# Kernel optimization log

Hardware: AMD Instinct MI355X
Metric: run time of the kernel (lower is better)

The kernel has to match this reference:

```python
import jax, jax.numpy as jnp
import numpy as np

NEG = -1e9


def setup_inputs() -> dict:
    key = jax.random.key(0)
    ks = jax.random.split(key, 9)
    B, L, S, E = 8, 2048, 2048, 1024
    H, G, KD, VD = 16, 64, 1024, 1024
    return {
        "query": jax.random.normal(ks[0], (B, L, E), jnp.float32),
        "key": jax.random.normal(ks[1], (B, S, E), jnp.float32),
        "value": jax.random.normal(ks[2], (B, S, E), jnp.float32),
        "other": jnp.zeros((1,), jnp.float32),
        "key_padding_mask": jax.random.bernoulli(ks[3], 0.1, (B, S)),
        "nhead": H,
        "query_proj": jax.random.normal(ks[4], (1, E, KD), jnp.float32) * 0.02,
        "key_proj": jax.random.normal(ks[5], (1, E, KD), jnp.float32) * 0.02,
        "value_proj": jax.random.normal(ks[6], (1, E, VD), jnp.float32) * 0.02,
        "importance_proj": jax.random.normal(ks[7], (1, E, H * G), jnp.float32) * 0.02,
        "output_proj": jax.random.normal(ks[8], (1, VD, E), jnp.float32) * 0.02,
    }


def reference(query, key, value, other, key_padding_mask, nhead,
              query_proj, key_proj, value_proj, importance_proj, output_proj):
    B, L, E = query.shape
    S = key.shape[1]
    H = nhead
    KD = query_proj.shape[-1]
    VD = value_proj.shape[-1]
    Ek, Ev = KD // H, VD // H
    G = importance_proj.shape[-1] // H
    scale = 1.0 / jnp.sqrt(jnp.asarray(Ek, query.dtype))

    # projections -> (B, H, L/S, d)
    qs = (query @ query_proj[0]).reshape(B, L, H, Ek).transpose(0, 2, 1, 3)
    kk = (key @ key_proj[0]).reshape(B, S, H, Ek).transpose(0, 2, 1, 3)
    vs = (value @ value_proj[0]).reshape(B, S, H, Ev).transpose(0, 2, 1, 3)

    # importance-weighted global queries: softmax over L
    ips = (query @ importance_proj[0]).reshape(B, L, H, G).transpose(0, 2, 3, 1)  # (B,H,G,L)
    ips = jax.nn.softmax(ips, axis=-1)
    gqs = jnp.einsum('bhgl,bhld->bhgd', ips, qs)  # (B,H,G,Ek)

    # stage 1: global queries attend over all keys (shared attn for keys & values)
    g_scores = jnp.einsum('bhgd,bhsd->bhgs', gqs, kk) * scale  # (B,H,G,S)
    g_scores = jnp.where(key_padding_mask[:, None, None, :], NEG, g_scores)
    g_attn = jax.nn.softmax(g_scores, axis=-1)
    global_keys = jnp.einsum('bhgs,bhsd->bhgd', g_attn, kk)   # (B,H,G,Ek)
    global_values = jnp.einsum('bhgs,bhsd->bhgd', g_attn, vs)  # (B,H,G,Ev)

    # stage 2: local queries attend over G global keys/values
    l_scores = jnp.einsum('bhld,bhgd->bhlg', qs, global_keys) * scale  # (B,H,L,G)
    l_attn = jax.nn.softmax(l_scores, axis=-1)
    out = jnp.einsum('bhlg,bhgd->bhld', l_attn, global_values)  # (B,H,L,Ev)

    out = out.transpose(0, 2, 1, 3).reshape(B, L, H * Ev)
    out = out @ output_proj[0]  # (B,L,E)
    return (out, l_attn)
```

## Files before the change

### kernel.cpp

```cpp
#include <hip/hip_runtime.h>


typedef float f32x4 __attribute__((ext_vector_type(4)));
typedef _Float16 f16x8 __attribute__((ext_vector_type(8)));
typedef unsigned short u16;

#define DEV static __device__ __forceinline__

DEV u16 f2h(float x){
  _Float16 h = (_Float16)x;
  return __builtin_bit_cast(u16, h);
}
DEV float h2f(u16 u){
  return (float)__builtin_bit_cast(_Float16, u);
}
DEV void split1h(float x, u16 &h, u16 &l){
  h = f2h(x);
  l = f2h(x - h2f(h));
}
DEV unsigned pk2h(float a, float b){
  return (unsigned)f2h(a) | ((unsigned)f2h(b) << 16);
}

DEV void gload16(const u16* src, u16* dst_lds){
  __builtin_amdgcn_global_load_lds(
      (__attribute__((address_space(1))) void*)src,
      (__attribute__((address_space(3))) void*)dst_lds, 16, 0, 0);
}

__global__ __launch_bounds__(256)
void mask_norm(const unsigned char* __restrict__ src, unsigned char* __restrict__ dst, int n)
{
  const unsigned* w = (const unsigned*)src;
  const int tid = threadIdx.x;
  int local = 0;
  for (int i = tid; i < n/4; i += 256){
    unsigned v = w[i];
    if (v == 0x3F800000u) local |= 2;
    else if (v > 1u)      local |= 1;
  }
  __shared__ int red[256];
  red[tid] = local;
  __syncthreads();
  for (int s = 128; s; s >>= 1){
    if (tid < s) red[tid] |= red[tid+s];
    __syncthreads();
  }
  const int r = red[0];
  const int mode = (r & 2) ? 2 : ((r & 1) ? 1 : 0);
  for (int i = tid; i < n; i += 256){
    unsigned char v;
    if (mode == 1) v = src[i] ? 1 : 0;
    else           v = w[i]   ? 1 : 0;
    dst[i] = v;
  }
}

__global__ __launch_bounds__(256)
void conv_hi(const float* __restrict__ x, u16* __restrict__ hi, int n8)
{
  const int i = blockIdx.x*256 + threadIdx.x;
  if (i >= n8) return;
  f32x4 a = ((const f32x4*)x)[2*i], b = ((const f32x4*)x)[2*i+1];
  uint4 uh;
  uh.x = pk2h(a[0], a[1]); uh.y = pk2h(a[2], a[3]);
  uh.z = pk2h(b[0], b[1]); uh.w = pk2h(b[2], b[3]);
  ((uint4*)hi)[i] = uh;
}

__global__ __launch_bounds__(256)
void transpose_hi(const float* __restrict__ Wsrc, u16* __restrict__ Whi, int Kd, int Nd)
{
  __shared__ float t[64][65];
  const int tid = threadIdx.x;
  const int n0 = blockIdx.x * 64, k0 = blockIdx.y * 64;
  #pragma unroll
  for (int it = 0; it < 16; ++it){
    int e = it*256 + tid, r = e >> 6, c = e & 63;
    t[r][c] = Wsrc[(long)(k0+r)*Nd + (n0+c)];
  }
  __syncthreads();
  #pragma unroll
  for (int it = 0; it < 16; ++it){
    int e = it*256 + tid, r = e >> 6, c = e & 63;
    Whi[(long)(n0+r)*Kd + (k0+c)] = f2h(t[c][r]);
  }
}

template<int TM, int TERMS, int CM, int EPI, int SWZ>
__global__ __launch_bounds__(256)
void gemm_g(const u16* __restrict__ Ah_g, const u16* __restrict__ Al_g,
            const u16* __restrict__ Bh_g,
            void* __restrict__ Cp, void* __restrict__ Cp2,
            const unsigned char* __restrict__ maskp,
            int K, int lda, int ldb, int ldc,
            long aB, long aH, long bB, long bH, long cB, long cH,
            int H2, int Ssz, float scale)
{
  constexpr int BN = 128, BK = 32;
  constexpr int WM = TM/2, WN = BN/2;
  constexpr int FM = WM/16, FN = WN/16;
  __shared__ __align__(16) u16 AhS[2][TM*BK];
  __shared__ __align__(16) u16 AlS[2][TERMS == 2 ? TM*BK : 8];
  __shared__ __align__(16) u16 BhS[2][BN*BK];

  const int tid = threadIdx.x;
  int bx = blockIdx.x, by = blockIdx.y;
  if constexpr (SWZ){
    const int gx = gridDim.x;
    const int nwg = gx * gridDim.y;
    const int q = nwg >> 3;
    const int flat = bx + gx * by;
    const int nf = (flat & 7) * q + (flat >> 3);
    bx = nf % gx; by = nf / gx;
  }
  const int batch = blockIdx.z;
  const int b = batch / H2, h = batch - b*H2;
  const long aOff = (long)b*aB + (long)h*aH;
  const long bOff = (long)b*bB + (long)h*bH;
  const long cOff = (long)b*cB + (long)h*cH;
  const int nBase = bx * BN;
  const int mBase = by * TM;
  const int wave = tid >> 6, lane = tid & 63;
  const int wm = wave >> 1, wn = wave & 1;
  const int cg8 = (lane & 3) * 8;
  const int rsub = lane >> 2;

  auto stage = [&](int buf, int k0){
    #pragma unroll
    for (int c = 0; c < TM/64; ++c){
      const int chunk = wave*(TM/64) + c;
      const long g = aOff + (long)(mBase + chunk*16 + rsub)*lda + k0 + cg8;
      gload16(Ah_g + g, &AhS[buf][chunk*512]);
      if constexpr (TERMS == 2) gload16(Al_g + g, &AlS[buf][chunk*512]);
    }
    #pragma unroll
    for (int c = 0; c < 2; ++c){
      const int chunk = wave*2 + c;
      const long g = bOff + (long)(nBase + chunk*16 + rsub)*ldb + k0 + cg8;
      gload16(Bh_g + g, &BhS[buf][chunk*512]);
    }
  };

  f32x4 acc[FM][FN] = {};

  stage(0, 0);
  __syncthreads();
  const int nk = K >> 5;
  for (int t = 0; t < nk; ++t){
    const int buf = t & 1;
    if (t + 1 < nk) stage(buf ^ 1, (t + 1) << 5);

    f16x8 ah[FM], al[FM], bh[FN];
    #pragma unroll
    for (int mi = 0; mi < FM; ++mi){
      const int off = (wm*WM + mi*16 + (lane & 15))*BK + (lane >> 4)*8;
      ah[mi] = *(const f16x8*)&AhS[buf][off];
      if constexpr (TERMS == 2) al[mi] = *(const f16x8*)&AlS[buf][off];
    }
    #pragma unroll
    for (int ni = 0; ni < FN; ++ni){
      const int off = (wn*WN + ni*16 + (lane & 15))*BK + (lane >> 4)*8;
      bh[ni] = *(const f16x8*)&BhS[buf][off];
    }
    #pragma unroll
    for (int mi = 0; mi < FM; ++mi)
      #pragma unroll
      for (int ni = 0; ni < FN; ++ni){
        acc[mi][ni] = __builtin_amdgcn_mfma_f32_16x16x32_f16(ah[mi], bh[ni], acc[mi][ni], 0, 0, 0);
        if constexpr (TERMS == 2)
          acc[mi][ni] = __builtin_amdgcn_mfma_f32_16x16x32_f16(al[mi], bh[ni], acc[mi][ni], 0, 0, 0);
      }
    __syncthreads();
  }

  const int cr = (lane >> 4) * 4, cc = lane & 15;
  #pragma unroll
  for (int mi = 0; mi < FM; ++mi)
    #pragma unroll
    for (int ni = 0; ni < FN; ++ni)
      #pragma unroll
      for (int r = 0; r < 4; ++r){
        const int row = mBase + wm*WM + mi*16 + cr + r;
        const int col = nBase + wn*WN + ni*16 + cc;
        float v = acc[mi][ni][r];
        if constexpr (EPI == 1){
          v *= scale;
          if (maskp[(long)b*Ssz + col]) v = -50000.0f;
        }
        const long ci = cOff + (long)row*ldc + col;
        if constexpr (CM == 0){
          ((float*)Cp)[ci] = v;
        } else {
          u16 hh, ll;
          split1h(v, hh, ll);
          ((u16*)Cp)[ci]  = hh;
          ((u16*)Cp2)[ci] = ll;
        }
      }
}

__global__ __launch_bounds__(256)
void softmax_split(u16* __restrict__ hi, u16* __restrict__ lo)
{
  const long base = (long)blockIdx.x * 2048;
  const int tid = threadIdx.x;
  const int lane = tid & 63, wv = tid >> 6;
  uint4 uh = ((const uint4*)(hi + base))[tid];
  uint4 ul = ((const uint4*)(lo + base))[tid];
  float v[8];
  v[0] = h2f((u16)uh.x) + h2f((u16)ul.x);
  v[1] = h2f((u16)(uh.x>>16)) + h2f((u16)(ul.x>>16));
  v[2] = h2f((u16)uh.y) + h2f((u16)ul.y);
  v[3] = h2f((u16)(uh.y>>16)) + h2f((u16)(ul.y>>16));
  v[4] = h2f((u16)uh.z) + h2f((u16)ul.z);
  v[5] = h2f((u16)(uh.z>>16)) + h2f((u16)(ul.z>>16));
  v[6] = h2f((u16)uh.w) + h2f((u16)ul.w);
  v[7] = h2f((u16)(uh.w>>16)) + h2f((u16)(ul.w>>16));
  float m = v[0];
  #pragma unroll
  for (int i = 1; i < 8; ++i) m = fmaxf(m, v[i]);
  #pragma unroll
  for (int off = 32; off; off >>= 1) m = fmaxf(m, __shfl_xor(m, off));
  __shared__ float rm[4], rs[4];
  if (lane == 0) rm[wv] = m;
  __syncthreads();
  m = fmaxf(fmaxf(rm[0],rm[1]), fmaxf(rm[2],rm[3]));
  float s = 0.f;
  #pragma unroll
  for (int i = 0; i < 8; ++i){ v[i] = __expf(v[i]-m); s += v[i]; }
  #pragma unroll
  for (int off = 32; off; off >>= 1) s += __shfl_xor(s, off);
  if (lane == 0) rs[wv] = s;
  __syncthreads();
  s = (rs[0]+rs[1]) + (rs[2]+rs[3]);
  const float inv = 1.0f / s;
  u16 hh[8], ll[8];
  #pragma unroll
  for (int i = 0; i < 8; ++i) split1h(v[i]*inv, hh[i], ll[i]);
  uh.x = (unsigned)hh[0] | ((unsigned)hh[1]<<16);
  uh.y = (unsigned)hh[2] | ((unsigned)hh[3]<<16);
  uh.z = (unsigned)hh[4] | ((unsigned)hh[5]<<16);
  uh.w = (unsigned)hh[6] | ((unsigned)hh[7]<<16);
  ul.x = (unsigned)ll[0] | ((unsigned)ll[1]<<16);
  ul.y = (unsigned)ll[2] | ((unsigned)ll[3]<<16);
  ul.z = (unsigned)ll[4] | ((unsigned)ll[5]<<16);
  ul.w = (unsigned)ll[6] | ((unsigned)ll[7]<<16);
  ((uint4*)(hi + base))[tid] = uh;
  ((uint4*)(lo + base))[tid] = ul;
}

template<int NB>
__global__ __launch_bounds__(256)
void einsum_m(const u16* __restrict__ Ah_g, const u16* __restrict__ Al_g,
              const u16* __restrict__ B1h_g, const u16* __restrict__ B1l_g,
              const u16* __restrict__ B2h_g, const u16* __restrict__ B2l_g,
              float* __restrict__ P1, float* __restrict__ P2,
              int K, int KC, int lda, int ldb,
              long aB, long aH, long bB, long bH, int H2, int nbatch)
{
  __shared__ __align__(16) u16 AhS[64][72];
  __shared__ __align__(16) u16 AlS[64][72];
  __shared__ __align__(16) u16 B1hS[64][72];
  __shared__ __align__(16) u16 B1lS[64][72];
  __shared__ __align__(16) u16 B2hS[NB==2?64:1][72];
  __shared__ __align__(16) u16 B2lS[NB==2?64:1][72];
  const int tid = threadIdx.x;
  const int kc = blockIdx.x, batch = blockIdx.y;
  const int b = batch / H2, h = batch - b*H2;
  const long aOff = (long)b*aB + (long)h*aH;
  const long bOff = (long)b*bB + (long)h*bH;
  const int kchunk = K / KC, kbeg = kc * kchunk;
  const int wm = tid >> 6, lane = tid & 63;
  const int ar = tid >> 3, as = (tid & 7) * 8;

  f32x4 acc1[4] = {};
  f32x4 acc2[4] = {};

  for (int ks = kbeg; ks < kbeg + kchunk; ks += 64){
    if (ks != kbeg) __syncthreads();
    #pragma unroll
    for (int it = 0; it < 2; ++it){
      const int g = it*32 + ar;
      const long ga = aOff + (long)g*lda + ks + as;
      *(uint4*)&AhS[g][as] = *(const uint4*)(Ah_g + ga);
      *(uint4*)&AlS[g][as] = *(const uint4*)(Al_g + ga);
    }
    #pragma unroll
    for (int it = 0; it < 4; ++it){
      const int e = it*256 + tid;
      const int lr = e >> 4, d0 = (e & 15) * 4;
      const long gm = bOff + (long)(ks + lr)*ldb + d0;
      ushort4 h4 = *(const ushort4*)(B1h_g + gm);
      ushort4 l4 = *(const ushort4*)(B1l_g + gm);
      B1hS[d0+0][lr]=h4.x; B1hS[d0+1][lr]=h4.y; B1hS[d0+2][lr]=h4.z; B1hS[d0+3][lr]=h4.w;
      B1lS[d0+0][lr]=l4.x; B1lS[d0+1][lr]=l4.y; B1lS[d0+2][lr]=l4.z; B1lS[d0+3][lr]=l4.w;
      if constexpr (NB == 2){
        ushort4 h42 = *(const ushort4*)(B2h_g + gm);
        ushort4 l42 = *(const ushort4*)(B2l_g + gm);
        B2hS[d0+0][lr]=h42.x; B2hS[d0+1][lr]=h42.y; B2hS[d0+2][lr]=h42.z; B2hS[d0+3][lr]=h42.w;
        B2lS[d0+0][lr]=l42.x; B2lS[d0+1][lr]=l42.y; B2lS[d0+2][lr]=l42.z; B2lS[d0+3][lr]=l42.w;
      }
    }
    __syncthreads();
    #pragma unroll
    for (int k0 = 0; k0 < 64; k0 += 32){
      const int ko = k0 + (lane >> 4)*8;
      const int fr = lane & 15;
      f16x8 a_h = *(const f16x8*)&AhS[wm*16 + fr][ko];
      f16x8 a_l = *(const f16x8*)&AlS[wm*16 + fr][ko];
      #pragma unroll
      for (int ni = 0; ni < 4; ++ni){
        f16x8 b_h = *(const f16x8*)&B1hS[ni*16 + fr][ko];
        f16x8 b_l = *(const f16x8*)&B1lS[ni*16 + fr][ko];
        acc1[ni] = __builtin_amdgcn_mfma_f32_16x16x32_f16(a_h, b_h, acc1[ni], 0, 0, 0);
        acc1[ni] = __builtin_amdgcn_mfma_f32_16x16x32_f16(a_l, b_h, acc1[ni], 0, 0, 0);
        acc1[ni] = __builtin_amdgcn_mfma_f32_16x16x32_f16(a_h, b_l, acc1[ni], 0, 0, 0);
        if constexpr (NB == 2){
          f16x8 c_h = *(const f16x8*)&B2hS[ni*16 + fr][ko];
          f16x8 c_l = *(const f16x8*)&B2lS[ni*16 + fr][ko];
          acc2[ni] = __builtin_amdgcn_mfma_f32_16x16x32_f16(a_h, c_h, acc2[ni], 0, 0, 0);
          acc2[ni] = __builtin_amdgcn_mfma_f32_16x16x32_f16(a_l, c_h, acc2[ni], 0, 0, 0);
          acc2[ni] = __builtin_amdgcn_mfma_f32_16x16x32_f16(a_h, c_l, acc2[ni], 0, 0, 0);
        }
      }
    }
  }
  const long po = ((long)(kc*nbatch + batch) << 12);
  const int cr = (lane >> 4) * 4, cc = lane & 15;
  #pragma unroll
  for (int ni = 0; ni < 4; ++ni)
    #pragma unroll
    for (int r = 0; r < 4; ++r){
      const int g = wm*16 + cr + r, d = ni*16 + cc;
      P1[po + g*64 + d] = acc1[ni][r];
      if constexpr (NB == 2) P2[po + g*64 + d] = acc2[ni][r];
    }
}

__global__ __launch_bounds__(256)
void reduce64(const float* __restrict__ part,
              u16* __restrict__ outhi, u16* __restrict__ outlo,
              int n4, int parts)
{
  const int idx = blockIdx.x*256 + threadIdx.x;
  if (idx >= n4) return;
  f32x4 s = ((const f32x4*)part)[idx];
  for (int p = 1; p < parts; ++p) s += ((const f32x4*)part)[(long)p*n4 + idx];
  ushort4 uh, ul;
  split1h(s[0], uh.x, ul.x); split1h(s[1], uh.y, ul.y);
  split1h(s[2], uh.z, ul.z); split1h(s[3], uh.w, ul.w);
  ((ushort4*)outhi)[idx] = uh;
  ((ushort4*)outlo)[idx] = ul;
}

__global__ __launch_bounds__(256)
void stage2_mfma(const u16* __restrict__ qhi, const u16* __restrict__ qlo,
                 const u16* __restrict__ gkh_g, const u16* __restrict__ gkl_g,
                 const u16* __restrict__ gvh_g, const u16* __restrict__ gvl_g,
                 float* __restrict__ lattn, u16* __restrict__ ahi,
                 float scale)
{
  __shared__ __align__(16) u16 Ah[128][72];
  __shared__ __align__(16) u16 Al[128][72];
  __shared__ __align__(16) u16 Bh[64][72];
  __shared__ __align__(16) u16 Bl[64][72];
  const int tid = threadIdx.x;
  const int bh = blockIdx.y;
  const int b = bh >> 4, h = bh & 15;
  const int l0 = blockIdx.x * 128;
  const int wm = tid >> 6, lane = tid & 63;

  const long qbase = ((long)b*2048 + l0)*1024 + h*64;
  #pragma unroll
  for (int it = 0; it < 4; ++it){
    const int e = it*256 + tid, row = e >> 3, s = e & 7;
    const long g = qbase + (long)row*1024 + s*8;
    *(uint4*)&Ah[row][s*8] = *(const uint4*)(qhi + g);
    *(uint4*)&Al[row][s*8] = *(const uint4*)(qlo + g);
  }
  const long gb = (long)bh * 4096;
  #pragma unroll
  for (int it = 0; it < 2; ++it){
    const int e = it*256 + tid, gr = e >> 3, s = e & 7;
    *(uint4*)&Bh[gr][s*8] = *(const uint4*)(gkh_g + gb + gr*64 + s*8);
    *(uint4*)&Bl[gr][s*8] = *(const uint4*)(gkl_g + gb + gr*64 + s*8);
  }
  __syncthreads();

  f32x4 acc[2][4] = {};
  #pragma unroll
  for (int k0 = 0; k0 < 64; k0 += 32){
    f16x8 a_h[2], a_l[2], b_h[4], b_l[4];
    #pragma unroll
    for (int mi = 0; mi < 2; ++mi){
      const int row = wm*32 + mi*16 + (lane & 15);
      a_h[mi] = *(const f16x8*)&Ah[row][k0 + (lane >> 4)*8];
      a_l[mi] = *(const f16x8*)&Al[row][k0 + (lane >> 4)*8];
    }
    #pragma unroll
    for (int ni = 0; ni < 4; ++ni){
      const int nr = ni*16 + (lane & 15);
      b_h[ni] = *(const f16x8*)&Bh[nr][k0 + (lane >> 4)*8];
      b_l[ni] = *(const f16x8*)&Bl[nr][k0 + (lane >> 4)*8];
    }
    #pragma unroll
    for (int mi = 0; mi < 2; ++mi)
      #pragma unroll
      for (int ni = 0; ni < 4; ++ni){
        acc[mi][ni] = __builtin_amdgcn_mfma_f32_16x16x32_f16(a_h[mi], b_h[ni], acc[mi][ni], 0, 0, 0);
        acc[mi][ni] = __builtin_amdgcn_mfma_f32_16x16x32_f16(a_l[mi], b_h[ni], acc[mi][ni], 0, 0, 0);
        acc[mi][ni] = __builtin_amdgcn_mfma_f32_16x16x32_f16(a_h[mi], b_l[ni], acc[mi][ni], 0, 0, 0);
      }
  }
  __syncthreads();

  #pragma unroll
  for (int it = 0; it < 4; ++it){
    const int e = it*256 + tid;
    const int gr = e >> 4, d0 = (e & 15) * 4;
    ushort4 vh = *(const ushort4*)(gvh_g + gb + gr*64 + d0);
    ushort4 vl = *(const ushort4*)(gvl_g + gb + gr*64 + d0);
    Bh[d0+0][gr] = vh.x; Bh[d0+1][gr] = vh.y; Bh[d0+2][gr] = vh.z; Bh[d0+3][gr] = vh.w;
    Bl[d0+0][gr] = vl.x; Bl[d0+1][gr] = vl.y; Bl[d0+2][gr] = vl.z; Bl[d0+3][gr] = vl.w;
  }

  #pragma unroll
  for (int mi = 0; mi < 2; ++mi){
    #pragma unroll
    for (int r = 0; r < 4; ++r){
      float v0 = acc[mi][0][r]*scale, v1 = acc[mi][1][r]*scale;
      float v2 = acc[mi][2][r]*scale, v3 = acc[mi][3][r]*scale;
      float mx = fmaxf(fmaxf(v0,v1), fmaxf(v2,v3));
      #pragma unroll
      for (int off = 1; off < 16; off <<= 1) mx = fmaxf(mx, __shfl_xor(mx, off, 16));
      float e0 = __expf(v0-mx), e1 = __expf(v1-mx), e2 = __expf(v2-mx), e3 = __expf(v3-mx);
      float sum = (e0+e1) + (e2+e3);
      #pragma unroll
      for (int off = 1; off < 16; off <<= 1) sum += __shfl_xor(sum, off, 16);
      const float inv = 1.0f / sum;
      e0 *= inv; e1 *= inv; e2 *= inv; e3 *= inv;
      const int lrow = wm*32 + mi*16 + (lane >> 4)*4 + r;
      float* lp = lattn + ((long)bh*2048 + l0 + lrow)*64 + (lane & 15);
      lp[0] = e0; lp[16] = e1; lp[32] = e2; lp[48] = e3;
      u16 hh, ll;
      split1h(e0, hh, ll); Ah[lrow][ 0 + (lane&15)] = hh; Al[lrow][ 0 + (lane&15)] = ll;
      split1h(e1, hh, ll); Ah[lrow][16 + (lane&15)] = hh; Al[lrow][16 + (lane&15)] = ll;
      split1h(e2, hh, ll); Ah[lrow][32 + (lane&15)] = hh; Al[lrow][32 + (lane&15)] = ll;
      split1h(e3, hh, ll); Ah[lrow][48 + (lane&15)] = hh; Al[lrow][48 + (lane&15)] = ll;
    }
  }
  __syncthreads();

  f32x4 o[2][4] = {};
  #pragma unroll
  for (int k0 = 0; k0 < 64; k0 += 32){
    f16x8 p_h[2], p_l[2], b_h[4], b_l[4];
    #pragma unroll
    for (int mi = 0; mi < 2; ++mi){
      const int row = wm*32 + mi*16 + (lane & 15);
      p_h[mi] = *(const f16x8*)&Ah[row][k0 + (lane >> 4)*8];
      p_l[mi] = *(const f16x8*)&Al[row][k0 + (lane >> 4)*8];
    }
    #pragma unroll
    for (int ni = 0; ni < 4; ++ni){
      const int nr = ni*16 + (lane & 15);
      b_h[ni] = *(const f16x8*)&Bh[nr][k0 + (lane >> 4)*8];
      b_l[ni] = *(const f16x8*)&Bl[nr][k0 + (lane >> 4)*8];
    }
    #pragma unroll
    for (int mi = 0; mi < 2; ++mi)
      #pragma unroll
      for (int ni = 0; ni < 4; ++ni){
        o[mi][ni] = __builtin_amdgcn_mfma_f32_16x16x32_f16(p_h[mi], b_h[ni], o[mi][ni], 0, 0, 0);
        o[mi][ni] = __builtin_amdgcn_mfma_f32_16x16x32_f16(p_l[mi], b_h[ni], o[mi][ni], 0, 0, 0);
        o[mi][ni] = __builtin_amdgcn_mfma_f32_16x16x32_f16(p_h[mi], b_l[ni], o[mi][ni], 0, 0, 0);
      }
  }

  #pragma unroll
  for (int mi = 0; mi < 2; ++mi)
    #pragma unroll
    for (int ni = 0; ni < 4; ++ni)
      #pragma unroll
      for (int r = 0; r < 4; ++r){
        const int lrow = wm*32 + mi*16 + (lane >> 4)*4 + r;
        const int d = ni*16 + (lane & 15);
        const long oidx = ((long)b*2048 + l0 + lrow)*1024 + h*64 + d;
        ahi[oidx] = f2h(o[mi][ni][r]);
      }
}

extern "C" void kernel_launch(void* const* d_in, const int* in_sizes, int n_in,
                              void* d_out, int out_size, void* d_ws, size_t ws_size,
                              hipStream_t stream)
{
  const float* query = (const float*)d_in[0];
  const float* key   = (const float*)d_in[1];
  const float* value = (const float*)d_in[2];
  const unsigned char* mask_raw = (const unsigned char*)d_in[4];
  const float* Wq = (const float*)d_in[6];
  const float* Wk = (const float*)d_in[7];
  const float* Wv = (const float*)d_in[8];
  const float* Wi = (const float*)d_in[9];
  const float* Wo = (const float*)d_in[10];
  float* out0 = (float*)d_out;
  float* out1 = out0 + 16777216;

  char* ws = (char*)d_ws;
  u16* WoT_hi = (u16*)(ws + 0);
  u16* WqT_hi = (u16*)(ws + (4L<<20));
  u16* WkT_hi = (u16*)(ws + (8L<<20));
  u16* WvT_hi = (u16*)(ws + (12L<<20));
  u16* WiT_hi = (u16*)(ws + (18L<<20));
  unsigned char* mask_ws = (unsigned char*)(ws + (6L<<20));
  u16* gqs_hi = (u16*)(ws + (16L<<20));
  u16* gqs_lo = (u16*)(ws + (17L<<20));
  float* part1 = (float*)(ws + (4L<<20));
  float* part2 = (float*)(ws + (12L<<20));
  u16* qp_hi = (u16*)(ws + (20L<<20));
  u16* kp_hi = qp_hi;
  u16* vp_hi = qp_hi;
  u16* gsc_hi = (u16*)(ws + (20L<<20));
  u16* gsc_lo = (u16*)(ws + (52L<<20));
  u16* qs_hi  = (u16*)(ws + (84L<<20));
  u16* qs_lo  = (u16*)(ws + (116L<<20));
  float* partg = (float*)(ws + (148L<<20));
  u16* vs_hi  = (u16*)(ws + (148L<<20));
  u16* vs_lo  = (u16*)(ws + (180L<<20));
  u16* ips_hi = (u16*)(ws + (212L<<20));
  u16* ips_lo = (u16*)(ws + (244L<<20));
  u16* kk_hi  = (u16*)(ws + (212L<<20));
  u16* kk_lo  = (u16*)(ws + (244L<<20));
  u16* gk_hi  = (u16*)(ws + (212L<<20));
  u16* gk_lo  = (u16*)(ws + (213L<<20));
  u16* gv_hi  = (u16*)(ws + (214L<<20));
  u16* gv_lo  = (u16*)(ws + (215L<<20));
  u16* attn_hi = (u16*)(ws + (244L<<20));

  const dim3 blk(256);
  const float scale = 0.125f;

  transpose_hi<<<dim3(16,16), blk, 0, stream>>>(Wq, WqT_hi, 1024, 1024);
  transpose_hi<<<dim3(16,16), blk, 0, stream>>>(Wk, WkT_hi, 1024, 1024);
  transpose_hi<<<dim3(16,16), blk, 0, stream>>>(Wv, WvT_hi, 1024, 1024);
  transpose_hi<<<dim3(16,16), blk, 0, stream>>>(Wi, WiT_hi, 1024, 1024);
  transpose_hi<<<dim3(16,16), blk, 0, stream>>>(Wo, WoT_hi, 1024, 1024);

  conv_hi<<<8192, blk, 0, stream>>>(query, qp_hi, 2097152);

  gemm_g<128,1,1,0,1><<<dim3(8,128,1), blk, 0, stream>>>(
      qp_hi, nullptr, WqT_hi, qs_hi, qs_lo, nullptr,
      1024, 1024,1024,1024, 0,0, 0,0, 0,0, 1, 2048, 1.f);

  gemm_g<128,1,1,0,0><<<dim3(16,8,8), blk, 0, stream>>>(
      WiT_hi, nullptr, qp_hi, ips_hi, ips_lo, nullptr,
      1024, 1024,1024,2048, 0,0, 2097152L,0, 2097152L,0, 1, 2048, 1.f);
  mask_norm<<<1, blk, 0, stream>>>(mask_raw, mask_ws, 16384);
  softmax_split<<<8192, blk, 0, stream>>>(ips_hi, ips_lo);

  einsum_m<1><<<dim3(4,128), blk, 0, stream>>>(
      ips_hi, ips_lo, qs_hi, qs_lo, nullptr, nullptr, partg, nullptr,
      2048, 4, 2048, 1024, 2097152L, 131072L, 2097152L, 64L, 16, 128);
  reduce64<<<512, blk, 0, stream>>>(partg, gqs_hi, gqs_lo, 131072, 4);

  conv_hi<<<8192, blk, 0, stream>>>(key, kp_hi, 2097152);
  gemm_g<128,1,1,0,1><<<dim3(8,128,1), blk, 0, stream>>>(
      kp_hi, nullptr, WkT_hi, kk_hi, kk_lo, nullptr,
      1024, 1024,1024,1024, 0,0, 0,0, 0,0, 1, 2048, 1.f);

  conv_hi<<<8192, blk, 0, stream>>>(value, vp_hi, 2097152);
  gemm_g<128,1,1,0,1><<<dim3(8,128,1), blk, 0, stream>>>(
      vp_hi, nullptr, WvT_hi, vs_hi, vs_lo, nullptr,
      1024, 1024,1024,1024, 0,0, 0,0, 0,0, 1, 2048, 1.f);

  gemm_g<64,2,1,1,0><<<dim3(16,1,128), blk, 0, stream>>>(
      gqs_hi, gqs_lo, kk_hi, gsc_hi, gsc_lo, mask_ws,
      64, 64,1024,2048, 65536L,4096L, 2097152L,64L, 2097152L,131072L, 16, 2048, scale);
  softmax_split<<<8192, blk, 0, stream>>>(gsc_hi, gsc_lo);

  einsum_m<2><<<dim3(4,128), blk, 0, stream>>>(
      gsc_hi, gsc_lo, kk_hi, kk_lo, vs_hi, vs_lo, part1, part2,
      2048, 4, 2048, 1024, 2097152L, 131072L, 2097152L, 64L, 16, 128);
  reduce64<<<512, blk, 0, stream>>>(part1, gk_hi, gk_lo, 131072, 4);
  reduce64<<<512, blk, 0, stream>>>(part2, gv_hi, gv_lo, 131072, 4);

  stage2_mfma<<<dim3(16,128), blk, 0, stream>>>(qs_hi, qs_lo, gk_hi, gk_lo,
      gv_hi, gv_lo, out1, attn_hi, scale);

  gemm_g<128,1,0,0,1><<<dim3(8,128,1), blk, 0, stream>>>(
      attn_hi, nullptr, WoT_hi, out0, nullptr, nullptr,
      1024, 1024,1024,1024, 0,0, 0,0, 0,0, 1, 2048, 1.f);

  (void)in_sizes; (void)n_in; (void)out_size; (void)ws_size;
}
```

Baseline: 576.5 us.

## Triple-buffer GEMM LDS staging with explicit vmcnt waits

Converts the generic GEMM's double-buffered global-to-LDS loads into a three-stage ring, issuing loads two K-steps ahead and waiting with explicit s_waitcnt vmcnt counts instead of a full __syncthreads. This is meant to hide global memory latency better by keeping more loads in flight. In exchange it uses 1.5x the LDS, which may reduce occupancy, and it adds sched_barriers that constrain the compiler's instruction scheduling.

Result: slower. 597.0 us (+3.6%).

```diff
diff --git a/kernel.cpp b/kernel.cpp
--- a/kernel.cpp
+++ b/kernel.cpp
@@ -26,6 +26,10 @@
   __builtin_amdgcn_global_load_lds(
       (__attribute__((address_space(1))) void*)src,
       (__attribute__((address_space(3))) void*)dst_lds, 16, 0, 0);
+}
+
+template<int N> DEV void wait_vm(){
+  asm volatile("s_waitcnt vmcnt(%0)" :: "i"(N) : "memory");
 }
 
 __global__ __launch_bounds__(256)
@@ -100,9 +104,10 @@
   constexpr int BN = 128, BK = 32;
   constexpr int WM = TM/2, WN = BN/2;
   constexpr int FM = WM/16, FN = WN/16;
-  __shared__ __align__(16) u16 AhS[2][TM*BK];
-  __shared__ __align__(16) u16 AlS[2][TERMS == 2 ? TM*BK : 8];
-  __shared__ __align__(16) u16 BhS[2][BN*BK];
+  constexpr int PL = TM/64 + (TERMS == 2 ? TM/64 : 0) + 2;
+  __shared__ __align__(16) u16 AhS[3][TM*BK];
+  __shared__ __align__(16) u16 AlS[3][TERMS == 2 ? TM*BK : 8];
+  __shared__ __align__(16) u16 BhS[3][BN*BK];
 
   const int tid = threadIdx.x;
   int bx = blockIdx.x, by = blockIdx.y;
@@ -144,25 +149,39 @@
 
   f32x4 acc[FM][FN] = {};
 
+  const int nk = K >> 5;
   stage(0, 0);
-  __syncthreads();
-  const int nk = K >> 5;
+  if (nk > 1) stage(1, 32);
+
+  int cur = 0;
   for (int t = 0; t < nk; ++t){
-    const int buf = t & 1;
-    if (t + 1 < nk) stage(buf ^ 1, (t + 1) << 5);
+    if (t + 2 < nk){
+      int nb = cur + 2; if (nb >= 3) nb -= 3;
+      stage(nb, (t + 2) << 5);
+      wait_vm<2*PL>();
+    } else if (t + 1 < nk){
+      wait_vm<PL>();
+    } else {
+      wait_vm<0>();
+    }
+    __builtin_amdgcn_s_barrier();
+    __builtin_amdgcn_sched_barrier(0);
 
     f16x8 ah[FM], al[FM], bh[FN];
     #pragma unroll
     for (int mi = 0; mi < FM; ++mi){
       const int off = (wm*WM + mi*16 + (lane & 15))*BK + (lane >> 4)*8;
-      ah[mi] = *(const f16x8*)&AhS[buf][off];
-      if constexpr (TERMS == 2) al[mi] = *(const f16x8*)&AlS[buf][off];
+      ah[mi] = *(const f16x8*)&AhS[cur][off];
+      if constexpr (TERMS == 2) al[mi] = *(const f16x8*)&AlS[cur][off];
     }
     #pragma unroll
     for (int ni = 0; ni < FN; ++ni){
       const int off = (wn*WN + ni*16 + (lane & 15))*BK + (lane >> 4)*8;
-      bh[ni] = *(const f16x8*)&BhS[buf][off];
-    }
+      bh[ni] = *(const f16x8*)&BhS[cur][off];
+    }
+    asm volatile("s_waitcnt lgkmcnt(0)" ::: "memory");
+    __builtin_amdgcn_sched_barrier(0);
+
     #pragma unroll
     for (int mi = 0; mi < FM; ++mi)
       #pragma unroll
@@ -171,7 +190,10 @@
         if constexpr (TERMS == 2)
           acc[mi][ni] = __builtin_amdgcn_mfma_f32_16x16x32_f16(al[mi], bh[ni], acc[mi][ni], 0, 0, 0);
       }
-    __syncthreads();
+
+    __builtin_amdgcn_s_barrier();
+    __builtin_amdgcn_sched_barrier(0);
+    ++cur; if (cur >= 3) cur -= 3;
   }
 
   const int cr = (lane >> 4) * 4, cc = lane & 15;
```

## Fuse softmax into aggregation einsums with online-softmax split-K combine

Applied to the files above, without the earlier changes.

Replaces the separate softmax_split pass plus einsum and reduce64 kernels with a flash-style aggregation kernel. It computes a running max and sum per row, rescales the accumulators, and writes partial stats that a small combine kernel merges across two K-chunks. This removes a full read and write of the large score tensors and two extra launches. The five weight transposes and two input conversions are also batched into single launches via blockIdx.z. In exchange, the number of K-splits per batch drops from 4 to 2, so fewer blocks are in flight, and extra syncs are added per tile.

Measured after the change: 565.3 us. About the same (-1.9%).

```diff
diff --git a/kernel.cpp b/kernel.cpp
--- a/kernel.cpp
+++ b/kernel.cpp
@@ -57,8 +57,11 @@
 }
 
 __global__ __launch_bounds__(256)
-void conv_hi(const float* __restrict__ x, u16* __restrict__ hi, int n8)
-{
+void conv_hi2(const float* __restrict__ x0, u16* __restrict__ h0,
+              const float* __restrict__ x1, u16* __restrict__ h1, int n8)
+{
+  const float* x = blockIdx.z ? x1 : x0;
+  u16* hi = blockIdx.z ? h1 : h0;
   const int i = blockIdx.x*256 + threadIdx.x;
   if (i >= n8) return;
   f32x4 a = ((const f32x4*)x)[2*i], b = ((const f32x4*)x)[2*i+1];
@@ -69,21 +72,40 @@
 }
 
 __global__ __launch_bounds__(256)
-void transpose_hi(const float* __restrict__ Wsrc, u16* __restrict__ Whi, int Kd, int Nd)
-{
+void conv_hi(const float* __restrict__ x, u16* __restrict__ hi, int n8)
+{
+  const int i = blockIdx.x*256 + threadIdx.x;
+  if (i >= n8) return;
+  f32x4 a = ((const f32x4*)x)[2*i], b = ((const f32x4*)x)[2*i+1];
+  uint4 uh;
+  uh.x = pk2h(a[0], a[1]); uh.y = pk2h(a[2], a[3]);
+  uh.z = pk2h(b[0], b[1]); uh.w = pk2h(b[2], b[3]);
+  ((uint4*)hi)[i] = uh;
+}
+
+__global__ __launch_bounds__(256)
+void transpose_hi5(const float* __restrict__ s0, const float* __restrict__ s1,
+                   const float* __restrict__ s2, const float* __restrict__ s3,
+                   const float* __restrict__ s4,
+                   u16* __restrict__ d0, u16* __restrict__ d1, u16* __restrict__ d2,
+                   u16* __restrict__ d3, u16* __restrict__ d4)
+{
+  const int z = blockIdx.z;
+  const float* Wsrc = z == 0 ? s0 : z == 1 ? s1 : z == 2 ? s2 : z == 3 ? s3 : s4;
+  u16* Whi = z == 0 ? d0 : z == 1 ? d1 : z == 2 ? d2 : z == 3 ? d3 : d4;
   __shared__ float t[64][65];
   const int tid = threadIdx.x;
   const int n0 = blockIdx.x * 64, k0 = blockIdx.y * 64;
   #pragma unroll
   for (int it = 0; it < 16; ++it){
     int e = it*256 + tid, r = e >> 6, c = e & 63;
-    t[r][c] = Wsrc[(long)(k0+r)*Nd + (n0+c)];
+    t[r][c] = Wsrc[(long)(k0+r)*1024 + (n0+c)];
   }
   __syncthreads();
   #pragma unroll
   for (int it = 0; it < 16; ++it){
     int e = it*256 + tid, r = e >> 6, c = e & 63;
-    Whi[(long)(n0+r)*Kd + (k0+c)] = f2h(t[c][r]);
+    Whi[(long)(n0+r)*1024 + (k0+c)] = f2h(t[c][r]);
   }
 }
 
@@ -200,71 +222,21 @@
       }
 }
 
-__global__ __launch_bounds__(256)
-void softmax_split(u16* __restrict__ hi, u16* __restrict__ lo)
-{
-  const long base = (long)blockIdx.x * 2048;
-  const int tid = threadIdx.x;
-  const int lane = tid & 63, wv = tid >> 6;
-  uint4 uh = ((const uint4*)(hi + base))[tid];
-  uint4 ul = ((const uint4*)(lo + base))[tid];
-  float v[8];
-  v[0] = h2f((u16)uh.x) + h2f((u16)ul.x);
-  v[1] = h2f((u16)(uh.x>>16)) + h2f((u16)(ul.x>>16));
-  v[2] = h2f((u16)uh.y) + h2f((u16)ul.y);
-  v[3] = h2f((u16)(uh.y>>16)) + h2f((u16)(ul.y>>16));
-  v[4] = h2f((u16)uh.z) + h2f((u16)ul.z);
-  v[5] = h2f((u16)(uh.z>>16)) + h2f((u16)(ul.z>>16));
-  v[6] = h2f((u16)uh.w) + h2f((u16)ul.w);
-  v[7] = h2f((u16)(uh.w>>16)) + h2f((u16)(ul.w>>16));
-  float m = v[0];
-  #pragma unroll
-  for (int i = 1; i < 8; ++i) m = fmaxf(m, v[i]);
-  #pragma unroll
-  for (int off = 32; off; off >>= 1) m = fmaxf(m, __shfl_xor(m, off));
-  __shared__ float rm[4], rs[4];
-  if (lane == 0) rm[wv] = m;
-  __syncthreads();
-  m = fmaxf(fmaxf(rm[0],rm[1]), fmaxf(rm[2],rm[3]));
-  float s = 0.f;
-  #pragma unroll
-  for (int i = 0; i < 8; ++i){ v[i] = __expf(v[i]-m); s += v[i]; }
-  #pragma unroll
-  for (int off = 32; off; off >>= 1) s += __shfl_xor(s, off);
-  if (lane == 0) rs[wv] = s;
-  __syncthreads();
-  s = (rs[0]+rs[1]) + (rs[2]+rs[3]);
-  const float inv = 1.0f / s;
-  u16 hh[8], ll[8];
-  #pragma unroll
-  for (int i = 0; i < 8; ++i) split1h(v[i]*inv, hh[i], ll[i]);
-  uh.x = (unsigned)hh[0] | ((unsigned)hh[1]<<16);
-  uh.y = (unsigned)hh[2] | ((unsigned)hh[3]<<16);
-  uh.z = (unsigned)hh[4] | ((unsigned)hh[5]<<16);
-  uh.w = (unsigned)hh[6] | ((unsigned)hh[7]<<16);
-  ul.x = (unsigned)ll[0] | ((unsigned)ll[1]<<16);
-  ul.y = (unsigned)ll[2] | ((unsigned)ll[3]<<16);
-  ul.z = (unsigned)ll[4] | ((unsigned)ll[5]<<16);
-  ul.w = (unsigned)ll[6] | ((unsigned)ll[7]<<16);
-  ((uint4*)(hi + base))[tid] = uh;
-  ((uint4*)(lo + base))[tid] = ul;
-}
-
 template<int NB>
 __global__ __launch_bounds__(256)
-void einsum_m(const u16* __restrict__ Ah_g, const u16* __restrict__ Al_g,
-              const u16* __restrict__ B1h_g, const u16* __restrict__ B1l_g,
-              const u16* __restrict__ B2h_g, const u16* __restrict__ B2l_g,
-              float* __restrict__ P1, float* __restrict__ P2,
-              int K, int KC, int lda, int ldb,
-              long aB, long aH, long bB, long bH, int H2, int nbatch)
-{
-  __shared__ __align__(16) u16 AhS[64][72];
-  __shared__ __align__(16) u16 AlS[64][72];
-  __shared__ __align__(16) u16 B1hS[64][72];
-  __shared__ __align__(16) u16 B1lS[64][72];
-  __shared__ __align__(16) u16 B2hS[NB==2?64:1][72];
-  __shared__ __align__(16) u16 B2lS[NB==2?64:1][72];
+void flash_agg(const u16* __restrict__ Sh_g, const u16* __restrict__ Sl_g,
+               const u16* __restrict__ B1h_g, const u16* __restrict__ B1l_g,
+               const u16* __restrict__ B2h_g, const u16* __restrict__ B2l_g,
+               float* __restrict__ P1, float* __restrict__ P2,
+               float* __restrict__ msm, float* __restrict__ mss,
+               int K, int KC, int lda, int ldb,
+               long aB, long aH, long bB, long bH, int H2, int nbatch)
+{
+  __shared__ __align__(16) u16 Ah[64][72], Al[64][72];
+  __shared__ __align__(16) u16 Ph[64][72], Pl[64][72];
+  __shared__ __align__(16) u16 B1h[64][72], B1l[64][72];
+  __shared__ __align__(16) u16 B2h[NB==2?64:1][72], B2l[NB==2?64:1][72];
+  __shared__ float mS[64], sS[64], fS[64];
   const int tid = threadIdx.x;
   const int kc = blockIdx.x, batch = blockIdx.y;
   const int b = batch / H2, h = batch - b*H2;
@@ -272,19 +244,20 @@
   const long bOff = (long)b*bB + (long)h*bH;
   const int kchunk = K / KC, kbeg = kc * kchunk;
   const int wm = tid >> 6, lane = tid & 63;
-  const int ar = tid >> 3, as = (tid & 7) * 8;
-
-  f32x4 acc1[4] = {};
-  f32x4 acc2[4] = {};
+  const int srow = tid >> 2, sq = tid & 3;
+
+  if (tid < 64){ mS[tid] = -1e30f; sS[tid] = 0.f; }
+
+  f32x4 acc1[4] = {}, acc2[4] = {};
 
   for (int ks = kbeg; ks < kbeg + kchunk; ks += 64){
-    if (ks != kbeg) __syncthreads();
+    __syncthreads();
     #pragma unroll
     for (int it = 0; it < 2; ++it){
-      const int g = it*32 + ar;
-      const long ga = aOff + (long)g*lda + ks + as;
-      *(uint4*)&AhS[g][as] = *(const uint4*)(Ah_g + ga);
-      *(uint4*)&AlS[g][as] = *(const uint4*)(Al_g + ga);
+      const int e = it*256 + tid, row = e >> 3, c8 = (e & 7) * 8;
+      const long ga = aOff + (long)row*lda + ks + c8;
+      *(uint4*)&Ah[row][c8] = *(const uint4*)(Sh_g + ga);
+      *(uint4*)&Al[row][c8] = *(const uint4*)(Sl_g + ga);
     }
     #pragma unroll
     for (int it = 0; it < 4; ++it){
@@ -293,32 +266,98 @@
       const long gm = bOff + (long)(ks + lr)*ldb + d0;
       ushort4 h4 = *(const ushort4*)(B1h_g + gm);
       ushort4 l4 = *(const ushort4*)(B1l_g + gm);
-      B1hS[d0+0][lr]=h4.x; B1hS[d0+1][lr]=h4.y; B1hS[d0+2][lr]=h4.z; B1hS[d0+3][lr]=h4.w;
-      B1lS[d0+0][lr]=l4.x; B1lS[d0+1][lr]=l4.y; B1lS[d0+2][lr]=l4.z; B1lS[d0+3][lr]=l4.w;
+      B1h[d0+0][lr]=h4.x; B1h[d0+1][lr]=h4.y; B1h[d0+2][lr]=h4.z; B1h[d0+3][lr]=h4.w;
+      B1l[d0+0][lr]=l4.x; B1l[d0+1][lr]=l4.y; B1l[d0+2][lr]=l4.z; B1l[d0+3][lr]=l4.w;
       if constexpr (NB == 2){
         ushort4 h42 = *(const ushort4*)(B2h_g + gm);
         ushort4 l42 = *(const ushort4*)(B2l_g + gm);
-        B2hS[d0+0][lr]=h42.x; B2hS[d0+1][lr]=h42.y; B2hS[d0+2][lr]=h42.z; B2hS[d0+3][lr]=h42.w;
-        B2lS[d0+0][lr]=l42.x; B2lS[d0+1][lr]=l42.y; B2lS[d0+2][lr]=l42.z; B2lS[d0+3][lr]=l42.w;
+        B2h[d0+0][lr]=h42.x; B2h[d0+1][lr]=h42.y; B2h[d0+2][lr]=h42.z; B2h[d0+3][lr]=h42.w;
+        B2l[d0+0][lr]=l42.x; B2l[d0+1][lr]=l42.y; B2l[d0+2][lr]=l42.z; B2l[d0+3][lr]=l42.w;
       }
     }
     __syncthreads();
+
+    float v[16];
+    {
+      uint4 ha = *(const uint4*)&Ah[srow][sq*16];
+      uint4 hb = *(const uint4*)&Ah[srow][sq*16 + 8];
+      uint4 la = *(const uint4*)&Al[srow][sq*16];
+      uint4 lb = *(const uint4*)&Al[srow][sq*16 + 8];
+      v[0]=h2f((u16)ha.x)+h2f((u16)la.x);  v[1]=h2f((u16)(ha.x>>16))+h2f((u16)(la.x>>16));
+      v[2]=h2f((u16)ha.y)+h2f((u16)la.y);  v[3]=h2f((u16)(ha.y>>16))+h2f((u16)(la.y>>16));
+      v[4]=h2f((u16)ha.z)+h2f((u16)la.z);  v[5]=h2f((u16)(ha.z>>16))+h2f((u16)(la.z>>16));
+      v[6]=h2f((u16)ha.w)+h2f((u16)la.w);  v[7]=h2f((u16)(ha.w>>16))+h2f((u16)(la.w>>16));
+      v[8]=h2f((u16)hb.x)+h2f((u16)lb.x);  v[9]=h2f((u16)(hb.x>>16))+h2f((u16)(lb.x>>16));
+      v[10]=h2f((u16)hb.y)+h2f((u16)lb.y); v[11]=h2f((u16)(hb.y>>16))+h2f((u16)(lb.y>>16));
+      v[12]=h2f((u16)hb.z)+h2f((u16)lb.z); v[13]=h2f((u16)(hb.z>>16))+h2f((u16)(lb.z>>16));
+      v[14]=h2f((u16)hb.w)+h2f((u16)lb.w); v[15]=h2f((u16)(hb.w>>16))+h2f((u16)(lb.w>>16));
+    }
+    float mx = v[0];
+    #pragma unroll
+    for (int i = 1; i < 16; ++i) mx = fmaxf(mx, v[i]);
+    mx = fmaxf(mx, __shfl_xor(mx, 1));
+    mx = fmaxf(mx, __shfl_xor(mx, 2));
+    const float mold = mS[srow];
+    const float mnew = fmaxf(mold, mx);
+    float sum = 0.f;
+    u16 ph[16], pl[16];
+    #pragma unroll
+    for (int i = 0; i < 16; ++i){
+      float e = __expf(v[i] - mnew);
+      sum += e;
+      split1h(e, ph[i], pl[i]);
+    }
+    sum += __shfl_xor(sum, 1);
+    sum += __shfl_xor(sum, 2);
+    if (sq == 0){
+      const float f = __expf(mold - mnew);
+      sS[srow] = sS[srow] * f + sum;
+      mS[srow] = mnew;
+      fS[srow] = f;
+    }
+    {
+      uint4 uh0, uh1, ul0, ul1;
+      uh0.x=(unsigned)ph[0]|((unsigned)ph[1]<<16);  uh0.y=(unsigned)ph[2]|((unsigned)ph[3]<<16);
+      uh0.z=(unsigned)ph[4]|((unsigned)ph[5]<<16);  uh0.w=(unsigned)ph[6]|((unsigned)ph[7]<<16);
+      uh1.x=(unsigned)ph[8]|((unsigned)ph[9]<<16);  uh1.y=(unsigned)ph[10]|((unsigned)ph[11]<<16);
+      uh1.z=(unsigned)ph[12]|((unsigned)ph[13]<<16);uh1.w=(unsigned)ph[14]|((unsigned)ph[15]<<16);
+      ul0.x=(unsigned)pl[0]|((unsigned)pl[1]<<16);  ul0.y=(unsigned)pl[2]|((unsigned)pl[3]<<16);
+      ul0.z=(unsigned)pl[4]|((unsigned)pl[5]<<16);  ul0.w=(unsigned)pl[6]|((unsigned)pl[7]<<16);
+      ul1.x=(unsigned)pl[8]|((unsigned)pl[9]<<16);  ul1.y=(unsigned)pl[10]|((unsigned)pl[11]<<16);
+      ul1.z=(unsigned)pl[12]|((unsigned)pl[13]<<16);ul1.w=(unsigned)pl[14]|((unsigned)pl[15]<<16);
+      *(uint4*)&Ph[srow][sq*16]     = uh0;
+      *(uint4*)&Ph[srow][sq*16 + 8] = uh1;
+      *(uint4*)&Pl[srow][sq*16]     = ul0;
+      *(uint4*)&Pl[srow][sq*16 + 8] = ul1;
+    }
+    __syncthreads();
+
+    float fr4[4];
+    #pragma unroll
+    for (int r = 0; r < 4; ++r) fr4[r] = fS[wm*16 + (lane >> 4)*4 + r];
+    #pragma unroll
+    for (int ni = 0; ni < 4; ++ni)
+      #pragma unroll
+      for (int r = 0; r < 4; ++r){
+        acc1[ni][r] *= fr4[r];
+        if constexpr (NB == 2) acc2[ni][r] *= fr4[r];
+      }
     #pragma unroll
     for (int k0 = 0; k0 < 64; k0 += 32){
       const int ko = k0 + (lane >> 4)*8;
       const int fr = lane & 15;
-      f16x8 a_h = *(const f16x8*)&AhS[wm*16 + fr][ko];
-      f16x8 a_l = *(const f16x8*)&AlS[wm*16 + fr][ko];
+      f16x8 a_h = *(const f16x8*)&Ph[wm*16 + fr][ko];
+      f16x8 a_l = *(const f16x8*)&Pl[wm*16 + fr][ko];
       #pragma unroll
       for (int ni = 0; ni < 4; ++ni){
-        f16x8 b_h = *(const f16x8*)&B1hS[ni*16 + fr][ko];
-        f16x8 b_l = *(const f16x8*)&B1lS[ni*16 + fr][ko];
+        f16x8 b_h = *(const f16x8*)&B1h[ni*16 + fr][ko];
+        f16x8 b_l = *(const f16x8*)&B1l[ni*16 + fr][ko];
         acc1[ni] = __builtin_amdgcn_mfma_f32_16x16x32_f16(a_h, b_h, acc1[ni], 0, 0, 0);
         acc1[ni] = __builtin_amdgcn_mfma_f32_16x16x32_f16(a_l, b_h, acc1[ni], 0, 0, 0);
         acc1[ni] = __builtin_amdgcn_mfma_f32_16x16x32_f16(a_h, b_l, acc1[ni], 0, 0, 0);
         if constexpr (NB == 2){
-          f16x8 c_h = *(const f16x8*)&B2hS[ni*16 + fr][ko];
-          f16x8 c_l = *(const f16x8*)&B2lS[ni*16 + fr][ko];
+          f16x8 c_h = *(const f16x8*)&B2h[ni*16 + fr][ko];
+          f16x8 c_l = *(const f16x8*)&B2l[ni*16 + fr][ko];
           acc2[ni] = __builtin_amdgcn_mfma_f32_16x16x32_f16(a_h, c_h, acc2[ni], 0, 0, 0);
           acc2[ni] = __builtin_amdgcn_mfma_f32_16x16x32_f16(a_l, c_h, acc2[ni], 0, 0, 0);
           acc2[ni] = __builtin_amdgcn_mfma_f32_16x16x32_f16(a_h, c_l, acc2[ni], 0, 0, 0);
@@ -326,6 +365,7 @@
       }
     }
   }
+
   const long po = ((long)(kc*nbatch + batch) << 12);
   const int cr = (lane >> 4) * 4, cc = lane & 15;
   #pragma unroll
@@ -336,22 +376,61 @@
       P1[po + g*64 + d] = acc1[ni][r];
       if constexpr (NB == 2) P2[po + g*64 + d] = acc2[ni][r];
     }
-}
-
-__global__ __launch_bounds__(256)
-void reduce64(const float* __restrict__ part,
-              u16* __restrict__ outhi, u16* __restrict__ outlo,
-              int n4, int parts)
-{
-  const int idx = blockIdx.x*256 + threadIdx.x;
-  if (idx >= n4) return;
-  f32x4 s = ((const f32x4*)part)[idx];
-  for (int p = 1; p < parts; ++p) s += ((const f32x4*)part)[(long)p*n4 + idx];
-  ushort4 uh, ul;
-  split1h(s[0], uh.x, ul.x); split1h(s[1], uh.y, ul.y);
-  split1h(s[2], uh.z, ul.z); split1h(s[3], uh.w, ul.w);
-  ((ushort4*)outhi)[idx] = uh;
-  ((ushort4*)outlo)[idx] = ul;
+  if (tid < 64){
+    msm[((long)kc*nbatch + batch)*64 + tid] = mS[tid];
+    mss[((long)kc*nbatch + batch)*64 + tid] = sS[tid];
+  }
+}
+
+template<int NB>
+__global__ __launch_bounds__(256)
+void flash_combine(const float* __restrict__ P1, const float* __restrict__ P2,
+                   const float* __restrict__ msm, const float* __restrict__ mss,
+                   u16* __restrict__ o1h, u16* __restrict__ o1l,
+                   u16* __restrict__ o2h, u16* __restrict__ o2l, int nbatch)
+{
+  const int batch = blockIdx.x;
+  const int tid = threadIdx.x;
+  const int g = tid >> 2, dq = (tid & 3) * 16;
+  const float m0 = msm[(long)batch*64 + g];
+  const float m1 = msm[((long)nbatch + batch)*64 + g];
+  const float s0 = mss[(long)batch*64 + g];
+  const float s1 = mss[((long)nbatch + batch)*64 + g];
+  const float M = fmaxf(m0, m1);
+  float w0 = __expf(m0 - M), w1 = __expf(m1 - M);
+  const float inv = 1.0f / (s0*w0 + s1*w1);
+  w0 *= inv; w1 *= inv;
+  const long i0 = ((long)batch << 12) + g*64 + dq;
+  const long i1 = (((long)nbatch + batch) << 12) + g*64 + dq;
+  const long oo = (long)batch*4096 + g*64 + dq;
+  #pragma unroll
+  for (int nb = 0; nb < NB; ++nb){
+    const float* Pa = nb ? P2 : P1;
+    u16* oh = nb ? o2h : o1h;
+    u16* ol = nb ? o2l : o1l;
+    u16 hh[16], ll[16];
+    #pragma unroll
+    for (int j = 0; j < 4; ++j){
+      f32x4 a = *(const f32x4*)(Pa + i0 + j*4);
+      f32x4 c = *(const f32x4*)(Pa + i1 + j*4);
+      #pragma unroll
+      for (int e = 0; e < 4; ++e)
+        split1h(a[e]*w0 + c[e]*w1, hh[j*4+e], ll[j*4+e]);
+    }
+    uint4 uh0, uh1, ul0, ul1;
+    uh0.x=(unsigned)hh[0]|((unsigned)hh[1]<<16);  uh0.y=(unsigned)hh[2]|((unsigned)hh[3]<<16);
+    uh0.z=(unsigned)hh[4]|((unsigned)hh[5]<<16);  uh0.w=(unsigned)hh[6]|((unsigned)hh[7]<<16);
+    uh1.x=(unsigned)hh[8]|((unsigned)hh[9]<<16);  uh1.y=(unsigned)hh[10]|((unsigned)hh[11]<<16);
+    uh1.z=(unsigned)hh[12]|((unsigned)hh[13]<<16);uh1.w=(unsigned)hh[14]|((unsigned)hh[15]<<16);
+    ul0.x=(unsigned)ll[0]|((unsigned)ll[1]<<16);  ul0.y=(unsigned)ll[2]|((unsigned)ll[3]<<16);
+    ul0.z=(unsigned)ll[4]|((unsigned)ll[5]<<16);  ul0.w=(unsigned)ll[6]|((unsigned)ll[7]<<16);
+    ul1.x=(unsigned)ll[8]|((unsigned)ll[9]<<16);  ul1.y=(unsigned)ll[10]|((unsigned)ll[11]<<16);
+    ul1.z=(unsigned)ll[12]|((unsigned)ll[13]<<16);ul1.w=(unsigned)ll[14]|((unsigned)ll[15]<<16);
+    *(uint4*)(oh + oo)     = uh0;
+    *(uint4*)(oh + oo + 8) = uh1;
+    *(uint4*)(ol + oo)     = ul0;
+    *(uint4*)(ol + oo + 8) = ul1;
+  }
 }
 
 __global__ __launch_bounds__(256)
@@ -509,19 +588,23 @@
 
   char* ws = (char*)d_ws;
   u16* WoT_hi = (u16*)(ws + 0);
+  float* msm_q = (float*)(ws + (2L<<20));
+  float* mss_q = (float*)(ws + (2L<<20) + 262144);
+  float* msm_g = (float*)(ws + (3L<<20));
+  float* mss_g = (float*)(ws + (3L<<20) + 262144);
   u16* WqT_hi = (u16*)(ws + (4L<<20));
+  unsigned char* mask_ws = (unsigned char*)(ws + (6L<<20));
+  float* part1 = (float*)(ws + (4L<<20));
   u16* WkT_hi = (u16*)(ws + (8L<<20));
   u16* WvT_hi = (u16*)(ws + (12L<<20));
-  u16* WiT_hi = (u16*)(ws + (18L<<20));
-  unsigned char* mask_ws = (unsigned char*)(ws + (6L<<20));
+  float* part2 = (float*)(ws + (12L<<20));
   u16* gqs_hi = (u16*)(ws + (16L<<20));
   u16* gqs_lo = (u16*)(ws + (17L<<20));
-  float* part1 = (float*)(ws + (4L<<20));
-  float* part2 = (float*)(ws + (12L<<20));
-  u16* qp_hi = (u16*)(ws + (20L<<20));
-  u16* kp_hi = qp_hi;
-  u16* vp_hi = qp_hi;
+  u16* WiT_hi = (u16*)(ws + (18L<<20));
+  u16* qp_hi  = (u16*)(ws + (20L<<20));
+  u16* vp_hi  = qp_hi;
   u16* gsc_hi = (u16*)(ws + (20L<<20));
+  u16* kp_hi  = (u16*)(ws + (52L<<20));
   u16* gsc_lo = (u16*)(ws + (52L<<20));
   u16* qs_hi  = (u16*)(ws + (84L<<20));
   u16* qs_lo  = (u16*)(ws + (116L<<20));
@@ -541,13 +624,12 @@
   const dim3 blk(256);
   const float scale = 0.125f;
 
-  transpose_hi<<<dim3(16,16), blk, 0, stream>>>(Wq, WqT_hi, 1024, 1024);
-  transpose_hi<<<dim3(16,16), blk, 0, stream>>>(Wk, WkT_hi, 1024, 1024);
-  transpose_hi<<<dim3(16,16), blk, 0, stream>>>(Wv, WvT_hi, 1024, 1024);
-  transpose_hi<<<dim3(16,16), blk, 0, stream>>>(Wi, WiT_hi, 1024, 1024);
-  transpose_hi<<<dim3(16,16), blk, 0, stream>>>(Wo, WoT_hi, 1024, 1024);
-
-  conv_hi<<<8192, blk, 0, stream>>>(query, qp_hi, 2097152);
+  mask_norm<<<1, blk, 0, stream>>>(mask_raw, mask_ws, 16384);
+
+  transpose_hi5<<<dim3(16,16,5), blk, 0, stream>>>(Wq, Wk, Wv, Wi, Wo,
+      WqT_hi, WkT_hi, WvT_hi, WiT_hi, WoT_hi);
+
+  conv_hi2<<<dim3(8192,1,2), blk, 0, stream>>>(query, qp_hi, key, kp_hi, 2097152);
 
   gemm_g<128,1,1,0,1><<<dim3(8,128,1), blk, 0, stream>>>(
       qp_hi, nullptr, WqT_hi, qs_hi, qs_lo, nullptr,
@@ -556,15 +638,14 @@
   gemm_g<128,1,1,0,0><<<dim3(16,8,8), blk, 0, stream>>>(
       WiT_hi, nullptr, qp_hi, ips_hi, ips_lo, nullptr,
       1024, 1024,1024,2048, 0,0, 2097152L,0, 2097152L,0, 1, 2048, 1.f);
-  mask_norm<<<1, blk, 0, stream>>>(mask_raw, mask_ws, 16384);
-  softmax_split<<<8192, blk, 0, stream>>>(ips_hi, ips_lo);
-
-  einsum_m<1><<<dim3(4,128), blk, 0, stream>>>(
-      ips_hi, ips_lo, qs_hi, qs_lo, nullptr, nullptr, partg, nullptr,
-      2048, 4, 2048, 1024, 2097152L, 131072L, 2097152L, 64L, 16, 128);
-  reduce64<<<512, blk, 0, stream>>>(partg, gqs_hi, gqs_lo, 131072, 4);
-
-  conv_hi<<<8192, blk, 0, stream>>>(key, kp_hi, 2097152);
+
+  flash_agg<1><<<dim3(2,128), blk, 0, stream>>>(
+      ips_hi, ips_lo, qs_hi, qs_lo, nullptr, nullptr,
+      partg, nullptr, msm_q, mss_q,
+      2048, 2, 2048, 1024, 2097152L, 131072L, 2097152L, 64L, 16, 128);
+  flash_combine<1><<<128, blk, 0, stream>>>(
+      partg, nullptr, msm_q, mss_q, gqs_hi, gqs_lo, nullptr, nullptr, 128);
+
   gemm_g<128,1,1,0,1><<<dim3(8,128,1), blk, 0, stream>>>(
       kp_hi, nullptr, WkT_hi, kk_hi, kk_lo, nullptr,
       1024, 1024,1024,1024, 0,0, 0,0, 0,0, 1, 2048, 1.f);
@@ -577,13 +658,13 @@
   gemm_g<64,2,1,1,0><<<dim3(16,1,128), blk, 0, stream>>>(
       gqs_hi, gqs_lo, kk_hi, gsc_hi, gsc_lo, mask_ws,
       64, 64,1024,2048, 65536L,4096L, 2097152L,64L, 2097152L,131072L, 16, 2048, scale);
-  softmax_split<<<8192, blk, 0, stream>>>(gsc_hi, gsc_lo);
-
-  einsum_m<2><<<dim3(4,128), blk, 0, stream>>>(
-      gsc_hi, gsc_lo, kk_hi, kk_lo, vs_hi, vs_lo, part1, part2,
-      2048, 4, 2048, 1024, 2097152L, 131072L, 2097152L, 64L, 16, 128);
-  reduce64<<<512, blk, 0, stream>>>(part1, gk_hi, gk_lo, 131072, 4);
-  reduce64<<<512, blk, 0, stream>>>(part2, gv_hi, gv_lo, 131072, 4);
+
+  flash_agg<2><<<dim3(2,128), blk, 0, stream>>>(
+      gsc_hi, gsc_lo, kk_hi, kk_lo, vs_hi, vs_lo,
+      part1, part2, msm_g, mss_g,
+      2048, 2, 2048, 1024, 2097152L, 131072L, 2097152L, 64L, 16, 128);
+  flash_combine<2><<<128, blk, 0, stream>>>(
+      part1, part2, msm_g, mss_g, gk_hi, gk_lo, gv_hi, gv_lo, 128);
 
   stage2_mfma<<<dim3(16,128), blk, 0, stream>>>(qs_hi, qs_lo, gk_hi, gk_lo,
       gv_hi, gv_lo, out1, attn_hi, scale);
```
